# Performance work log

Measured on AMD Instinct MI355X. Metric: run time of the kernel, lower is better.

Reference implementation:

```python
import jax, jax.numpy as jnp
import numpy as np

N_NODES = 100000
N_EDGES = 1600000


def _add_self_loops(edge_index, num_nodes):
    loop = jnp.arange(num_nodes, dtype=edge_index.dtype)
    src = jnp.concatenate([edge_index[0], loop])
    dst = jnp.concatenate([edge_index[1], loop])
    return src, dst


def _gcn_conv(x, src, dst, W, b, num_nodes):
    # PyG GCNConv: h = x W, then symmetric-normalized scatter-add aggregation.
    h = x @ W  # [N, F_out]
    ones = jnp.ones(src.shape[0], dtype=x.dtype)
    deg = jax.ops.segment_sum(ones, dst, num_segments=num_nodes)  # in-degree incl. self-loops
    dinv = jnp.where(deg > 0, jax.lax.rsqrt(deg), 0.0)
    norm = dinv[src] * dinv[dst]  # [E]
    msg = h[src] * norm[:, None]  # irregular gather, [E, F_out]
    out = jax.ops.segment_sum(msg, dst, num_segments=num_nodes)  # scatter-add, [N, F_out]
    return out + b


def setup_inputs() -> dict:
    key = jax.random.key(0)
    ks = jax.random.split(key, 4)
    x = jax.random.uniform(ks[0], (N_NODES, 32), dtype=jnp.float32)
    edge_index = jax.random.randint(ks[1], (2, N_EDGES), 0, N_NODES, dtype=jnp.int64)
    W1 = jax.random.normal(ks[2], (32, 64), dtype=jnp.float32) * (1.0 / np.sqrt(32))
    b1 = jnp.zeros((64,), dtype=jnp.float32)
    W2 = jax.random.normal(ks[3], (64, 128), dtype=jnp.float32) * (1.0 / np.sqrt(64))
    b2 = jnp.zeros((128,), dtype=jnp.float32)
    return {"x": x, "edge_index": edge_index, "W1": W1, "b1": b1, "W2": W2, "b2": b2}


def reference(x, edge_index, W1, b1, W2, b2):
    num_nodes = x.shape[0]
    src, dst = _add_self_loops(edge_index, num_nodes)
    h = _gcn_conv(x, src, dst, W1, b1, num_nodes)
    h = jax.nn.relu(h)
    out = _gcn_conv(h, src, dst, W2, b2, num_nodes)
    return out
```

## Files before the change

kernel.cpp:

```cpp
#include <hip/hip_runtime.h>
#include <hip/hip_fp16.h>

static inline int cdiv(int a, int b) { return (a + b - 1) / b; }

#define NWORD 25600
#define HC    64

struct h2x2 { __half2 a; __half2 b; };

__global__ __launch_bounds__(1024) void k_hist(const int* __restrict__ dst, int E, int N, int chunk,
                                               unsigned char* __restrict__ rank8,
                                               unsigned char* __restrict__ Mb) {
    __shared__ unsigned int cnt[NWORD];
    int c = blockIdx.x;
    for (int i = threadIdx.x; i < NWORD; i += 1024) cnt[i] = 0;
    __syncthreads();
    int ebeg = c * chunk;
    int eend = min(E, ebeg + chunk);
    for (int e = ebeg + threadIdx.x; e < eend; e += 1024) {
        int d = dst[e];
        int sh = (d & 3) * 8;
        unsigned int old = atomicAdd(&cnt[d >> 2], 1u << sh);
        rank8[e] = (unsigned char)((old >> sh) & 0xFF);
    }
    __syncthreads();
    unsigned int* Mrow = (unsigned int*)(Mb + (size_t)c * N);
    int nw = N >> 2;
    for (int i = threadIdx.x; i < nw; i += 1024) Mrow[i] = cnt[i];
}

__global__ __launch_bounds__(256) void k_degpre(const unsigned char* __restrict__ Mb, int N,
                                                unsigned char* __restrict__ pre8,
                                                int* __restrict__ deg, float* __restrict__ dinv) {
    int i = blockIdx.x * 256 + threadIdx.x;
    if (i >= (N >> 2)) return;
    unsigned int s0 = 0, s1 = 0, s2 = 0, s3 = 0;
#pragma unroll
    for (int c = 0; c < HC; ++c) {
        unsigned int w = *(const unsigned int*)(Mb + (size_t)c * N + 4 * i);
        *(unsigned int*)(pre8 + (size_t)c * N + 4 * i) = s0 | (s1 << 8) | (s2 << 16) | (s3 << 24);
        s0 += w & 0xFF; s1 += (w >> 8) & 0xFF; s2 += (w >> 16) & 0xFF; s3 += (w >> 24) & 0xFF;
    }
    ((int4*)deg)[i] = make_int4((int)s0, (int)s1, (int)s2, (int)s3);
    ((float4*)dinv)[i] = make_float4(rsqrtf((float)(s0 + 1)), rsqrtf((float)(s1 + 1)),
                                     rsqrtf((float)(s2 + 1)), rsqrtf((float)(s3 + 1)));
}

#define SCAN_BS 1024

__global__ __launch_bounds__(SCAN_BS) void k_blocksum(const int* __restrict__ deg, int N, int* __restrict__ bsum) {
    __shared__ int s[SCAN_BS];
    int t = threadIdx.x;
    int i = blockIdx.x * SCAN_BS + t;
    s[t] = (i < N) ? deg[i] : 0;
    __syncthreads();
    for (int off = SCAN_BS / 2; off > 0; off >>= 1) {
        if (t < off) s[t] += s[t + off];
        __syncthreads();
    }
    if (t == 0) bsum[blockIdx.x] = s[0];
}

__global__ __launch_bounds__(128) void k_scan_bsums(const int* __restrict__ bsum, int NB, int* __restrict__ boff) {
    __shared__ int s[128];
    int t = threadIdx.x;
    int v = (t < NB) ? bsum[t] : 0;
    s[t] = v;
    __syncthreads();
    for (int off = 1; off < 128; off <<= 1) {
        int u = (t >= off) ? s[t - off] : 0;
        __syncthreads();
        s[t] += u;
        __syncthreads();
    }
    if (t < NB) boff[t] = s[t] - v;
}

__global__ __launch_bounds__(SCAN_BS) void k_scan_final(const int* __restrict__ deg, int N,
                                                        const int* __restrict__ boff,
                                                        int* __restrict__ offsets, int E) {
    __shared__ int s[SCAN_BS];
    int t = threadIdx.x;
    int i = blockIdx.x * SCAN_BS + t;
    int v = (i < N) ? deg[i] : 0;
    s[t] = v;
    __syncthreads();
    for (int off = 1; off < SCAN_BS; off <<= 1) {
        int u = (t >= off) ? s[t - off] : 0;
        __syncthreads();
        s[t] += u;
        __syncthreads();
    }
    if (i < N) offsets[i] = boff[blockIdx.x] + s[t] - v;
    if (blockIdx.x == 0 && t == 0) offsets[N] = E;
}

__global__ __launch_bounds__(256) void k_scatter(const int* __restrict__ ei, int E, int N, int chunk,
                                                 const int* __restrict__ offsets,
                                                 const unsigned char* __restrict__ pre8,
                                                 const unsigned char* __restrict__ rank8,
                                                 int* __restrict__ csr_src) {
    int t = blockIdx.x * 256 + threadIdx.x;
    int e0 = t * 4;
    if (e0 + 3 < E) {
        int4 s4 = *(const int4*)(ei + e0);
        int4 d4 = *(const int4*)(ei + E + e0);
        uchar4 r4 = *(const uchar4*)(rank8 + e0);
        int c0 = (e0 + 0) / chunk, c1 = (e0 + 1) / chunk, c2 = (e0 + 2) / chunk, c3 = (e0 + 3) / chunk;
        int o0 = offsets[d4.x], o1 = offsets[d4.y], o2 = offsets[d4.z], o3 = offsets[d4.w];
        int p0 = (int)pre8[(size_t)c0 * N + d4.x];
        int p1 = (int)pre8[(size_t)c1 * N + d4.y];
        int p2 = (int)pre8[(size_t)c2 * N + d4.z];
        int p3 = (int)pre8[(size_t)c3 * N + d4.w];
        csr_src[o0 + p0 + (int)r4.x] = s4.x;
        csr_src[o1 + p1 + (int)r4.y] = s4.y;
        csr_src[o2 + p2 + (int)r4.z] = s4.z;
        csr_src[o3 + p3 + (int)r4.w] = s4.w;
    } else {
        for (int e = e0; e < E; ++e) {
            int s = ei[e];
            int d = ei[E + e];
            int c = e / chunk;
            int pos = offsets[d] + (int)pre8[(size_t)c * N + d] + (int)rank8[e];
            csr_src[pos] = s;
        }
    }
}

__global__ __launch_bounds__(256) void k_cast32(const float* __restrict__ x, const float* __restrict__ dinv,
                                                __half* __restrict__ xh, int N) {
    int i = blockIdx.x * 256 + threadIdx.x;
    if (i >= N * 8) return;
    int g = i >> 3;
    float di = dinv[g];
    float4 v = ((const float4*)x)[i];
    __half2 h0 = __floats2half2_rn(v.x * di, v.y * di);
    __half2 h1 = __floats2half2_rn(v.z * di, v.w * di);
    ((__half2*)xh)[2 * i] = h0;
    ((__half2*)xh)[2 * i + 1] = h1;
}

template <int F>
__global__ __launch_bounds__(256) void k_agg(const __half* __restrict__ feat,
                                             const int* __restrict__ offsets,
                                             const int* __restrict__ csr_src,
                                             const float* __restrict__ dinv,
                                             float* __restrict__ out, int N) {
    constexpr int L = F / 4;
    int t = blockIdx.x * 256 + threadIdx.x;
    int g = t / L;
    int q = t % L;
    if (g >= N) return;
    const h2x2* f4 = (const h2x2*)feat;
    int beg = offsets[g];
    int end = offsets[g + 1];
    float di = dinv[g];
    float4 acc;
    {
        h2x2 w = f4[(size_t)g * L + q];
        float2 lo = __half22float2(w.a);
        float2 hi = __half22float2(w.b);
        acc = make_float4(lo.x, lo.y, hi.x, hi.y);
    }
    int e = beg;
    for (; e + 4 <= end; e += 4) {
        int s0 = csr_src[e + 0], s1 = csr_src[e + 1], s2 = csr_src[e + 2], s3 = csr_src[e + 3];
        h2x2 w0 = f4[(size_t)s0 * L + q];
        h2x2 w1 = f4[(size_t)s1 * L + q];
        h2x2 w2 = f4[(size_t)s2 * L + q];
        h2x2 w3 = f4[(size_t)s3 * L + q];
        float2 a0 = __half22float2(w0.a), b0 = __half22float2(w0.b);
        float2 a1 = __half22float2(w1.a), b1 = __half22float2(w1.b);
        float2 a2 = __half22float2(w2.a), b2 = __half22float2(w2.b);
        float2 a3 = __half22float2(w3.a), b3 = __half22float2(w3.b);
        acc.x += (a0.x + a1.x) + (a2.x + a3.x);
        acc.y += (a0.y + a1.y) + (a2.y + a3.y);
        acc.z += (b0.x + b1.x) + (b2.x + b3.x);
        acc.w += (b0.y + b1.y) + (b2.y + b3.y);
    }
    for (; e < end; ++e) {
        h2x2 w = f4[(size_t)csr_src[e] * L + q];
        float2 lo = __half22float2(w.a);
        float2 hi = __half22float2(w.b);
        acc.x += lo.x; acc.y += lo.y; acc.z += hi.x; acc.w += hi.y;
    }
    ((float4*)out)[(size_t)g * L + q] = make_float4(acc.x * di, acc.y * di, acc.z * di, acc.w * di);
}

__global__ __launch_bounds__(256) void k_gemm1(const float* __restrict__ A, const float* __restrict__ W,
                                               const float* __restrict__ b, const float* __restrict__ dinv,
                                               __half* __restrict__ out, int N) {
    __shared__ float sA[32][68];
    __shared__ float sW[32][64];
    int tid = threadIdx.x;
    int row0 = blockIdx.x * 64;

    {
        const float4* Wv = (const float4*)W;
        float4* sWv = (float4*)&sW[0][0];
        sWv[tid] = Wv[tid];
        sWv[tid + 256] = Wv[tid + 256];
    }
    {
        int row = tid >> 2;
        int gr = row0 + row;
        int kq = (tid & 3) * 4;
#pragma unroll
        for (int i = 0; i < 2; ++i) {
            int k0 = kq + 16 * i;
            float4 v = (gr < N) ? *(const float4*)(A + (size_t)gr * 32 + k0)
                                : make_float4(0.f, 0.f, 0.f, 0.f);
            sA[k0 + 0][row] = v.x;
            sA[k0 + 1][row] = v.y;
            sA[k0 + 2][row] = v.z;
            sA[k0 + 3][row] = v.w;
        }
    }
    __syncthreads();

    int tm = tid & 15, tn = tid >> 4;
    float acc[4][4];
#pragma unroll
    for (int i = 0; i < 4; ++i) {
        float4 bb = *(const float4*)(b + tn * 4);
        acc[i][0] = bb.x; acc[i][1] = bb.y; acc[i][2] = bb.z; acc[i][3] = bb.w;
    }
#pragma unroll 4
    for (int k = 0; k < 32; ++k) {
        float4 a = *(const float4*)&sA[k][tm * 4];
        float4 w = *(const float4*)&sW[k][tn * 4];
        float av[4] = {a.x, a.y, a.z, a.w};
        float wv[4] = {w.x, w.y, w.z, w.w};
#pragma unroll
        for (int i = 0; i < 4; ++i)
#pragma unroll
            for (int j = 0; j < 4; ++j) acc[i][j] = fmaf(av[i], wv[j], acc[i][j]);
    }
#pragma unroll
    for (int i = 0; i < 4; ++i) {
        int row = row0 + tm * 4 + i;
        if (row < N) {
            float di = dinv[row];
            __half2 p0 = __floats2half2_rn(fmaxf(acc[i][0], 0.f) * di, fmaxf(acc[i][1], 0.f) * di);
            __half2 p1 = __floats2half2_rn(fmaxf(acc[i][2], 0.f) * di, fmaxf(acc[i][3], 0.f) * di);
            __half2* op = (__half2*)(out + (size_t)row * 64);
            op[tn * 2] = p0;
            op[tn * 2 + 1] = p1;
        }
    }
}

__global__ __launch_bounds__(256) void k_gemm2(const float* __restrict__ A, const float* __restrict__ W,
                                               const float* __restrict__ b, float* __restrict__ out, int N) {
    __shared__ float sA[64][68];
    __shared__ float sW[64][128];
    int tid = threadIdx.x;
    int row0 = blockIdx.x * 64;

    {
        const float4* Wv = (const float4*)W;
        float4* sWv = (float4*)&sW[0][0];
#pragma unroll
        for (int i = 0; i < 8; ++i) sWv[tid + 256 * i] = Wv[tid + 256 * i];
    }
    {
        int row = tid >> 2;
        int gr = row0 + row;
        int kq = (tid & 3) * 4;
#pragma unroll
        for (int i = 0; i < 4; ++i) {
            int k0 = kq + 16 * i;
            float4 v = (gr < N) ? *(const float4*)(A + (size_t)gr * 64 + k0)
                                : make_float4(0.f, 0.f, 0.f, 0.f);
            sA[k0 + 0][row] = v.x;
            sA[k0 + 1][row] = v.y;
            sA[k0 + 2][row] = v.z;
            sA[k0 + 3][row] = v.w;
        }
    }
    __syncthreads();

    int tm = tid & 15, tn = tid >> 4;
    float acc[4][8];
    {
        float4 b0 = *(const float4*)(b + tn * 8);
        float4 b1 = *(const float4*)(b + tn * 8 + 4);
#pragma unroll
        for (int i = 0; i < 4; ++i) {
            acc[i][0] = b0.x; acc[i][1] = b0.y; acc[i][2] = b0.z; acc[i][3] = b0.w;
            acc[i][4] = b1.x; acc[i][5] = b1.y; acc[i][6] = b1.z; acc[i][7] = b1.w;
        }
    }
#pragma unroll 4
    for (int k = 0; k < 64; ++k) {
        float4 a = *(const float4*)&sA[k][tm * 4];
        float4 w0 = *(const float4*)&sW[k][tn * 8];
        float4 w1 = *(const float4*)&sW[k][tn * 8 + 4];
        float av[4] = {a.x, a.y, a.z, a.w};
        float wv[8] = {w0.x, w0.y, w0.z, w0.w, w1.x, w1.y, w1.z, w1.w};
#pragma unroll
        for (int i = 0; i < 4; ++i)
#pragma unroll
            for (int j = 0; j < 8; ++j) acc[i][j] = fmaf(av[i], wv[j], acc[i][j]);
    }
#pragma unroll
    for (int i = 0; i < 4; ++i) {
        int row = row0 + tm * 4 + i;
        if (row < N) {
            *(float4*)(out + (size_t)row * 128 + tn * 8) =
                make_float4(acc[i][0], acc[i][1], acc[i][2], acc[i][3]);
            *(float4*)(out + (size_t)row * 128 + tn * 8 + 4) =
                make_float4(acc[i][4], acc[i][5], acc[i][6], acc[i][7]);
        }
    }
}

extern "C" void kernel_launch(void* const* d_in, const int* in_sizes, int n_in,
                              void* d_out, int out_size, void* d_ws, size_t ws_size,
                              hipStream_t stream) {
    const float* x  = (const float*)d_in[0];
    const int*   ei = (const int*)d_in[1];
    const float* W1 = (const float*)d_in[2];
    const float* b1 = (const float*)d_in[3];
    const float* W2 = (const float*)d_in[4];
    const float* b2 = (const float*)d_in[5];
    float* out = (float*)d_out;

    const int N = in_sizes[0] / 32;
    const int E = in_sizes[1] / 2;
    const int chunk = cdiv(E, HC);

    char* ws = (char*)d_ws;
    size_t off = 0;
    auto walloc = [&](size_t bytes) -> void* {
        void* p = ws + off;
        off = (off + bytes + 255) & ~(size_t)255;
        return p;
    };
    unsigned char* Mb      = (unsigned char*) walloc((size_t)HC * N);
    unsigned char* pre8    = (unsigned char*) walloc((size_t)HC * N);
    int*           deg     = (int*)           walloc((size_t)N * 4);
    float*         dinv    = (float*)         walloc((size_t)N * 4);
    int*           offsets = (int*)           walloc((size_t)(N + 4) * 4);
    int*           bsum    = (int*)           walloc(128 * 4);
    int*           boff    = (int*)           walloc(128 * 4);
    unsigned char* rank8   = (unsigned char*) walloc((size_t)E);
    int*           csr_src = (int*)           walloc((size_t)E * 4);
    __half*        xh      = (__half*)        walloc((size_t)N * 32 * 2);
    float*         a1      = (float*)         walloc((size_t)N * 32 * 4);
    __half*        h2h     = (__half*)        walloc((size_t)N * 64 * 2);
    float*         a2      = (float*)         walloc((size_t)N * 64 * 4);
    (void)ws_size; (void)n_in; (void)out_size;

    k_hist<<<HC, 1024, 0, stream>>>(ei + E, E, N, chunk, rank8, Mb);
    k_degpre<<<cdiv(N / 4, 256), 256, 0, stream>>>(Mb, N, pre8, deg, dinv);

    const int NB = cdiv(N, SCAN_BS);
    k_blocksum<<<NB, SCAN_BS, 0, stream>>>(deg, N, bsum);
    k_scan_bsums<<<1, 128, 0, stream>>>(bsum, NB, boff);
    k_scan_final<<<NB, SCAN_BS, 0, stream>>>(deg, N, boff, offsets, E);

    k_cast32<<<cdiv(N * 8, 256), 256, 0, stream>>>(x, dinv, xh, N);
    k_scatter<<<cdiv(E, 1024), 256, 0, stream>>>(ei, E, N, chunk, offsets, pre8, rank8, csr_src);

    k_agg<32><<<cdiv(N * 8, 256), 256, 0, stream>>>(xh, offsets, csr_src, dinv, a1, N);
    k_gemm1<<<cdiv(N, 64), 256, 0, stream>>>(a1, W1, b1, dinv, h2h, N);

    k_agg<64><<<cdiv(N * 16, 256), 256, 0, stream>>>(h2h, offsets, csr_src, dinv, a2, N);
    k_gemm2<<<cdiv(N, 64), 256, 0, stream>>>(a2, W2, b2, out, N);
}
```

Before: 167.2 us.

## Replace random CSR scatter with bucketed two-pass partition; widen aggregation loads

```diff
diff --git a/kernel.cpp b/kernel.cpp
--- a/kernel.cpp
+++ b/kernel.cpp
@@ -5,8 +5,10 @@
 
 #define NWORD 25600
 #define HC    64
-
-struct h2x2 { __half2 a; __half2 b; };
+#define NBLK  256
+#define BKT_SHIFT 12
+
+struct h2x4 { __half2 a, b, c, d; };
 
 __global__ __launch_bounds__(1024) void k_hist(const int* __restrict__ dst, int E, int N, int chunk,
                                                unsigned char* __restrict__ rank8,
@@ -95,35 +97,75 @@
     if (blockIdx.x == 0 && t == 0) offsets[N] = E;
 }
 
-__global__ __launch_bounds__(256) void k_scatter(const int* __restrict__ ei, int E, int N, int chunk,
-                                                 const int* __restrict__ offsets,
-                                                 const unsigned char* __restrict__ pre8,
-                                                 const unsigned char* __restrict__ rank8,
-                                                 int* __restrict__ csr_src) {
+__global__ __launch_bounds__(256) void k_pos(const int* __restrict__ ei, int E, int N, int chunk, int epb, int nbuk,
+                                             const int* __restrict__ offsets,
+                                             const unsigned char* __restrict__ pre8,
+                                             const unsigned char* __restrict__ rank8,
+                                             int* __restrict__ posarr, int* __restrict__ cnt) {
+    __shared__ int h[512];
+    int blk = blockIdx.x;
+    for (int b = threadIdx.x; b < nbuk; b += 256) h[b] = 0;
+    __syncthreads();
+    int beg = blk * epb;
+    int end = min(E, beg + epb);
+    const int* dst = ei + E;
+    int e = beg + threadIdx.x;
+    for (; e + 768 < end; e += 1024) {
+        int e0 = e, e1 = e + 256, e2 = e + 512, e3 = e + 768;
+        int d0 = dst[e0], d1 = dst[e1], d2 = dst[e2], d3 = dst[e3];
+        int c0 = e0 / chunk, c1 = e1 / chunk, c2 = e2 / chunk, c3 = e3 / chunk;
+        int o0 = offsets[d0], o1 = offsets[d1], o2 = offsets[d2], o3 = offsets[d3];
+        int q0 = (int)pre8[(size_t)c0 * N + d0] + (int)rank8[e0];
+        int q1 = (int)pre8[(size_t)c1 * N + d1] + (int)rank8[e1];
+        int q2 = (int)pre8[(size_t)c2 * N + d2] + (int)rank8[e2];
+        int q3 = (int)pre8[(size_t)c3 * N + d3] + (int)rank8[e3];
+        int p0 = o0 + q0, p1 = o1 + q1, p2 = o2 + q2, p3 = o3 + q3;
+        posarr[e0] = p0; posarr[e1] = p1; posarr[e2] = p2; posarr[e3] = p3;
+        atomicAdd(&h[p0 >> BKT_SHIFT], 1);
+        atomicAdd(&h[p1 >> BKT_SHIFT], 1);
+        atomicAdd(&h[p2 >> BKT_SHIFT], 1);
+        atomicAdd(&h[p3 >> BKT_SHIFT], 1);
+    }
+    for (; e < end; e += 256) {
+        int d = dst[e];
+        int c = e / chunk;
+        int p = offsets[d] + (int)pre8[(size_t)c * N + d] + (int)rank8[e];
+        posarr[e] = p;
+        atomicAdd(&h[p >> BKT_SHIFT], 1);
+    }
+    __syncthreads();
+    for (int b = threadIdx.x; b < nbuk; b += 256) cnt[(size_t)b * NBLK + blk] = h[b];
+}
+
+__global__ __launch_bounds__(256) void k_part2(const int* __restrict__ ei, int E, int epb, int nbuk,
+                                               const int* __restrict__ cbase,
+                                               const int* __restrict__ posarr,
+                                               int2* __restrict__ pairs) {
+    __shared__ int lb[512];
+    int blk = blockIdx.x;
+    for (int b = threadIdx.x; b < nbuk; b += 256) lb[b] = cbase[(size_t)b * NBLK + blk];
+    __syncthreads();
+    int beg = blk * epb;
+    int end = min(E, beg + epb);
+    for (int e = beg + threadIdx.x; e < end; e += 256) {
+        int s = ei[e];
+        int p = posarr[e];
+        int slot = atomicAdd(&lb[p >> BKT_SHIFT], 1);
+        pairs[slot] = make_int2(s, p);
+    }
+}
+
+__global__ __launch_bounds__(256) void k_scat2(const int2* __restrict__ pairs, int E,
+                                               int* __restrict__ csr_src) {
     int t = blockIdx.x * 256 + threadIdx.x;
-    int e0 = t * 4;
-    if (e0 + 3 < E) {
-        int4 s4 = *(const int4*)(ei + e0);
-        int4 d4 = *(const int4*)(ei + E + e0);
-        uchar4 r4 = *(const uchar4*)(rank8 + e0);
-        int c0 = (e0 + 0) / chunk, c1 = (e0 + 1) / chunk, c2 = (e0 + 2) / chunk, c3 = (e0 + 3) / chunk;
-        int o0 = offsets[d4.x], o1 = offsets[d4.y], o2 = offsets[d4.z], o3 = offsets[d4.w];
-        int p0 = (int)pre8[(size_t)c0 * N + d4.x];
-        int p1 = (int)pre8[(size_t)c1 * N + d4.y];
-        int p2 = (int)pre8[(size_t)c2 * N + d4.z];
-        int p3 = (int)pre8[(size_t)c3 * N + d4.w];
-        csr_src[o0 + p0 + (int)r4.x] = s4.x;
-        csr_src[o1 + p1 + (int)r4.y] = s4.y;
-        csr_src[o2 + p2 + (int)r4.z] = s4.z;
-        csr_src[o3 + p3 + (int)r4.w] = s4.w;
-    } else {
-        for (int e = e0; e < E; ++e) {
-            int s = ei[e];
-            int d = ei[E + e];
-            int c = e / chunk;
-            int pos = offsets[d] + (int)pre8[(size_t)c * N + d] + (int)rank8[e];
-            csr_src[pos] = s;
-        }
+    int e0 = t * 2;
+    if (e0 + 1 < E) {
+        int4 two = ((const int4*)pairs)[t];
+        csr_src[two.y] = two.x;
+        csr_src[two.w] = two.z;
+    } else if (e0 < E) {
+        int2 pr = pairs[e0];
+        csr_src[pr.y] = pr.x;
     }
 }
 
@@ -146,45 +188,60 @@
                                              const int* __restrict__ csr_src,
                                              const float* __restrict__ dinv,
                                              float* __restrict__ out, int N) {
-    constexpr int L = F / 4;
+    constexpr int L = F / 8;
     int t = blockIdx.x * 256 + threadIdx.x;
     int g = t / L;
     int q = t % L;
     if (g >= N) return;
-    const h2x2* f4 = (const h2x2*)feat;
+    const h2x4* f8 = (const h2x4*)feat;
     int beg = offsets[g];
     int end = offsets[g + 1];
     float di = dinv[g];
-    float4 acc;
-    {
-        h2x2 w = f4[(size_t)g * L + q];
-        float2 lo = __half22float2(w.a);
-        float2 hi = __half22float2(w.b);
-        acc = make_float4(lo.x, lo.y, hi.x, hi.y);
+    float acc[8];
+    {
+        h2x4 w = f8[(size_t)g * L + q];
+        float2 p0 = __half22float2(w.a), p1 = __half22float2(w.b);
+        float2 p2 = __half22float2(w.c), p3 = __half22float2(w.d);
+        acc[0] = p0.x; acc[1] = p0.y; acc[2] = p1.x; acc[3] = p1.y;
+        acc[4] = p2.x; acc[5] = p2.y; acc[6] = p3.x; acc[7] = p3.y;
     }
     int e = beg;
     for (; e + 4 <= end; e += 4) {
         int s0 = csr_src[e + 0], s1 = csr_src[e + 1], s2 = csr_src[e + 2], s3 = csr_src[e + 3];
-        h2x2 w0 = f4[(size_t)s0 * L + q];
-        h2x2 w1 = f4[(size_t)s1 * L + q];
-        h2x2 w2 = f4[(size_t)s2 * L + q];
-        h2x2 w3 = f4[(size_t)s3 * L + q];
-        float2 a0 = __half22float2(w0.a), b0 = __half22float2(w0.b);
-        float2 a1 = __half22float2(w1.a), b1 = __half22float2(w1.b);
-        float2 a2 = __half22float2(w2.a), b2 = __half22float2(w2.b);
-        float2 a3 = __half22float2(w3.a), b3 = __half22float2(w3.b);
-        acc.x += (a0.x + a1.x) + (a2.x + a3.x);
-        acc.y += (a0.y + a1.y) + (a2.y + a3.y);
-        acc.z += (b0.x + b1.x) + (b2.x + b3.x);
-        acc.w += (b0.y + b1.y) + (b2.y + b3.y);
+        h2x4 w0 = f8[(size_t)s0 * L + q];
+        h2x4 w1 = f8[(size_t)s1 * L + q];
+        h2x4 w2 = f8[(size_t)s2 * L + q];
+        h2x4 w3 = f8[(size_t)s3 * L + q];
+        float2 u;
+        u = __half22float2(w0.a); acc[0] += u.x; acc[1] += u.y;
+        u = __half22float2(w0.b); acc[2] += u.x; acc[3] += u.y;
+        u = __half22float2(w0.c); acc[4] += u.x; acc[5] += u.y;
+        u = __half22float2(w0.d); acc[6] += u.x; acc[7] += u.y;
+        u = __half22float2(w1.a); acc[0] += u.x; acc[1] += u.y;
+        u = __half22float2(w1.b); acc[2] += u.x; acc[3] += u.y;
+        u = __half22float2(w1.c); acc[4] += u.x; acc[5] += u.y;
+        u = __half22float2(w1.d); acc[6] += u.x; acc[7] += u.y;
+        u = __half22float2(w2.a); acc[0] += u.x; acc[1] += u.y;
+        u = __half22float2(w2.b); acc[2] += u.x; acc[3] += u.y;
+        u = __half22float2(w2.c); acc[4] += u.x; acc[5] += u.y;
+        u = __half22float2(w2.d); acc[6] += u.x; acc[7] += u.y;
+        u = __half22float2(w3.a); acc[0] += u.x; acc[1] += u.y;
+        u = __half22float2(w3.b); acc[2] += u.x; acc[3] += u.y;
+        u = __half22float2(w3.c); acc[4] += u.x; acc[5] += u.y;
+        u = __half22float2(w3.d); acc[6] += u.x; acc[7] += u.y;
     }
     for (; e < end; ++e) {
-        h2x2 w = f4[(size_t)csr_src[e] * L + q];
-        float2 lo = __half22float2(w.a);
-        float2 hi = __half22float2(w.b);
-        acc.x += lo.x; acc.y += lo.y; acc.z += hi.x; acc.w += hi.y;
-    }
-    ((float4*)out)[(size_t)g * L + q] = make_float4(acc.x * di, acc.y * di, acc.z * di, acc.w * di);
+        h2x4 w = f8[(size_t)csr_src[e] * L + q];
+        float2 u;
+        u = __half22float2(w.a); acc[0] += u.x; acc[1] += u.y;
+        u = __half22float2(w.b); acc[2] += u.x; acc[3] += u.y;
+        u = __half22float2(w.c); acc[4] += u.x; acc[5] += u.y;
+        u = __half22float2(w.d); acc[6] += u.x; acc[7] += u.y;
+    }
+    float4 o0 = make_float4(acc[0] * di, acc[1] * di, acc[2] * di, acc[3] * di);
+    float4 o1 = make_float4(acc[4] * di, acc[5] * di, acc[6] * di, acc[7] * di);
+    ((float4*)out)[(size_t)g * (F / 4) + q * 2] = o0;
+    ((float4*)out)[(size_t)g * (F / 4) + q * 2 + 1] = o1;
 }
 
 __global__ __launch_bounds__(256) void k_gemm1(const float* __restrict__ A, const float* __restrict__ W,
@@ -329,6 +386,9 @@
     const int N = in_sizes[0] / 32;
     const int E = in_sizes[1] / 2;
     const int chunk = cdiv(E, HC);
+    const int epb = cdiv(E, NBLK);
+    const int nbuk = cdiv(E, 1 << BKT_SHIFT);
+    const int clen = nbuk * NBLK;
 
     char* ws = (char*)d_ws;
     size_t off = 0;
@@ -345,6 +405,10 @@
     int*           bsum    = (int*)           walloc(128 * 4);
     int*           boff    = (int*)           walloc(128 * 4);
     unsigned char* rank8   = (unsigned char*) walloc((size_t)E);
+    int*           posarr  = (int*)           walloc((size_t)E * 4);
+    int*           cnt     = (int*)           walloc((size_t)(clen + 4) * 4);
+    int*           cbase   = (int*)           walloc((size_t)(clen + 4) * 4);
+    int2*          pairs   = (int2*)          walloc((size_t)E * 8);
     int*           csr_src = (int*)           walloc((size_t)E * 4);
     __half*        xh      = (__half*)        walloc((size_t)N * 32 * 2);
     float*         a1      = (float*)         walloc((size_t)N * 32 * 4);
@@ -361,11 +425,18 @@
     k_scan_final<<<NB, SCAN_BS, 0, stream>>>(deg, N, boff, offsets, E);
 
     k_cast32<<<cdiv(N * 8, 256), 256, 0, stream>>>(x, dinv, xh, N);
-    k_scatter<<<cdiv(E, 1024), 256, 0, stream>>>(ei, E, N, chunk, offsets, pre8, rank8, csr_src);
-
-    k_agg<32><<<cdiv(N * 8, 256), 256, 0, stream>>>(xh, offsets, csr_src, dinv, a1, N);
+
+    k_pos<<<NBLK, 256, 0, stream>>>(ei, E, N, chunk, epb, nbuk, offsets, pre8, rank8, posarr, cnt);
+    const int NB2 = cdiv(clen, SCAN_BS);
+    k_blocksum<<<NB2, SCAN_BS, 0, stream>>>(cnt, clen, bsum);
+    k_scan_bsums<<<1, 128, 0, stream>>>(bsum, NB2, boff);
+    k_scan_final<<<NB2, SCAN_BS, 0, stream>>>(cnt, clen, boff, cbase, E);
+    k_part2<<<NBLK, 256, 0, stream>>>(ei, E, epb, nbuk, cbase, posarr, pairs);
+    k_scat2<<<cdiv(E, 512), 256, 0, stream>>>(pairs, E, csr_src);
+
+    k_agg<32><<<cdiv(N * 4, 256), 256, 0, stream>>>(xh, offsets, csr_src, dinv, a1, N);
     k_gemm1<<<cdiv(N, 64), 256, 0, stream>>>(a1, W1, b1, dinv, h2h, N);
 
-    k_agg<64><<<cdiv(N * 16, 256), 256, 0, stream>>>(h2h, offsets, csr_src, dinv, a2, N);
+    k_agg<64><<<cdiv(N * 8, 256), 256, 0, stream>>>(h2h, offsets, csr_src, dinv, a2, N);
     k_gemm2<<<cdiv(N, 64), 256, 0, stream>>>(a2, W2, b2, out, N);
 }
```

Result: slower. 187.1 us (+11.9%).
